# Kernel optimization log

Measured on AMD Instinct MI355X. Metric: run time of the kernel, lower is better.

## Reference

```python
import jax, jax.numpy as jnp
import numpy as np

B = 65536
NQ = 8
NL = 3
FEAT = 64 * 3 * 3 + NQ  # 584


def _conv(x, w, b):
    # x: (B,C,H,W), w: (O,I,3,3), padding=1 -> SAME
    y = jax.lax.conv_general_dilated(
        x, w, window_strides=(1, 1), padding='SAME',
        dimension_numbers=('NCHW', 'OIHW', 'NCHW'))
    return y + b[None, :, None, None]


def _maxpool2(x):
    return jax.lax.reduce_window(
        x, -jnp.inf, jax.lax.max, (1, 1, 2, 2), (1, 1, 2, 2), 'VALID')


def _quantum_sim(x, qp):
    # x: (B,NQ); qp: (NL,NQ,3). Within a layer, qubit q depends only on its own
    # previous state (tanh term), so vectorize over qubits and scan over layers.
    x_next = jnp.roll(x, -1, axis=1)  # x[:, (q+1) % NQ]

    def step(q_state, rot):  # rot: (NQ,3)
        new = jnp.sin(rot[:, 0] * x) * jnp.cos(rot[:, 1] * x_next) \
              + jnp.tanh(rot[:, 2] * q_state)
        return new, None

    q0 = jnp.zeros_like(x)
    qf, _ = jax.lax.scan(step, q0, qp)
    return qf


def setup_inputs() -> dict:
    key = jax.random.key(0)
    ks = jax.random.split(key, 16)

    def w(k, shape, fan_in):
        lim = 1.0 / np.sqrt(fan_in)
        return jax.random.uniform(k, shape, jnp.float32, -lim, lim)

    return {
        'board_state': jax.random.normal(ks[0], (B, 3, 6, 6), jnp.float32),
        'target_positions': jax.random.randint(ks[1], (4, 2), 0, 6).astype(jnp.int64),
        'conv1_w': w(ks[2], (16, 3, 3, 3), 3 * 9), 'conv1_b': w(ks[3], (16,), 3 * 9),
        'conv2_w': w(ks[4], (32, 16, 3, 3), 16 * 9), 'conv2_b': w(ks[5], (32,), 16 * 9),
        'conv3_w': w(ks[6], (64, 32, 3, 3), 32 * 9), 'conv3_b': w(ks[7], (64,), 32 * 9),
        'quantum_params': jax.random.normal(ks[8], (NL, NQ, 3), jnp.float32),
        'pt_w1': w(ks[9], (FEAT, 128), FEAT), 'pt_b1': w(ks[9], (128,), FEAT),
        'pt_w2': w(ks[10], (128, 64), 128), 'pt_b2': w(ks[10], (64,), 128),
        'pt_w3': w(ks[11], (64, 2), 64), 'pt_b3': w(ks[11], (2,), 64),
        'cf_w1': w(ks[12], (FEAT, 64), FEAT), 'cf_b1': w(ks[12], (64,), FEAT),
        'cf_w2': w(ks[13], (64, 1), 64), 'cf_b2': w(ks[13], (1,), 64),
    }


def reference(board_state, target_positions,
              conv1_w, conv1_b, conv2_w, conv2_b, conv3_w, conv3_b,
              quantum_params,
              pt_w1, pt_b1, pt_w2, pt_b2, pt_w3, pt_b3,
              cf_w1, cf_b1, cf_w2, cf_b2):
    b = board_state.shape[0]
    h = jax.nn.relu(_conv(board_state, conv1_w, conv1_b))   # (B,16,6,6)
    h = jax.nn.relu(_conv(h, conv2_w, conv2_b))             # (B,32,6,6)
    h = _maxpool2(h)                                        # (B,32,3,3)
    h = jax.nn.relu(_conv(h, conv3_w, conv3_b))             # (B,64,3,3)
    conv_flat = h.reshape(b, -1)                            # (B,576)

    board_flat = board_state.reshape(b, -1)
    q_feat = _quantum_sim(board_flat[:, :NQ], quantum_params)  # (B,NQ)

    feats = jnp.concatenate([conv_flat, q_feat], axis=1)    # (B,584)

    # piece-type head (Dropout is identity in eval)
    t = jax.nn.relu(feats @ pt_w1 + pt_b1)
    t = jax.nn.relu(t @ pt_w2 + pt_b2)
    type_logits = t @ pt_w3 + pt_b3
    type_probs = jax.nn.softmax(type_logits, axis=1)        # (B,2)

    # confidence head
    c = jax.nn.relu(feats @ cf_w1 + cf_b1)
    confidence = jax.nn.sigmoid(c @ cf_w2 + cf_b2)          # (B,1)

    # target_positions never affect the math (pos_encoding unused in torch source);
    # the same probs/confidence are reported for every position.
    return jnp.concatenate([type_probs, confidence], axis=1)  # (B,3)
```

## Files before the change

### kernel.cpp

```cpp
#include <hip/hip_runtime.h>

typedef _Float16 h8 __attribute__((ext_vector_type(8)));
typedef _Float16 h4 __attribute__((ext_vector_type(4)));
typedef float f32x4 __attribute__((ext_vector_type(4)));

union HU { _Float16 h; unsigned short u; };
__device__ __forceinline__ unsigned short f2h(float f) { HU x; x.h = (_Float16)f; return x.u; }
__device__ __forceinline__ float h2f(unsigned short u) { HU x; x.u = u; return (float)x.h; }

#define MFMA16(a, b, c) __builtin_amdgcn_mfma_f32_16x16x32_f16((a), (b), (c), 0, 0, 0)

__global__ void k_prep(const float* __restrict__ w1, const float* __restrict__ w2,
                       const float* __restrict__ w3,
                       const float* __restrict__ ptw1, const float* __restrict__ cfw1,
                       const float* __restrict__ ptw2, const float* __restrict__ ptw3,
                       const float* __restrict__ cfw2,
                       unsigned short* __restrict__ w1f,
                       unsigned short* __restrict__ w2f,
                       unsigned short* __restrict__ w3f,
                       unsigned short* __restrict__ w1hd,
                       unsigned short* __restrict__ w2hd,
                       unsigned short* __restrict__ w3hd) {
    int gid = blockIdx.x * 256 + threadIdx.x;
    int gs = gridDim.x * 256;
    for (int e = gid; e < 512; e += gs) {
        int j = e & 7, lane = e >> 3;
        int k = ((lane >> 4) * 8) + j, oc = lane & 15;
        float v = 0.f;
        if (k < 27) { int t = k / 3, ic = k % 3; v = w1[oc * 27 + ic * 9 + t]; }
        w1f[e] = f2h(v);
    }
    for (int e = gid; e < 9216; e += gs) {
        int j = e & 7, lane = (e >> 3) & 63, fo = e >> 9;
        int ot = fo & 1, t = fo >> 1;
        int k = ((lane >> 4) * 8) + j, oc = ot * 16 + (lane & 15);
        float v = (k < 16) ? w2[oc * 144 + k * 9 + t] : 0.f;
        w2f[e] = f2h(v);
    }
    for (int e = gid; e < 18432; e += gs) {
        int j = e & 7, lane = (e >> 3) & 63, fo = e >> 9;
        int oti = fo & 1, t = (fo >> 1) % 9, otp = (fo >> 1) / 9;
        int ic = ((lane >> 4) * 8) + j, oc = (otp * 2 + oti) * 16 + (lane & 15);
        w3f[e] = f2h(w3[oc * 288 + ic * 9 + t]);
    }
    for (int s = gid; s < 608 * 192; s += gs) {
        int k = s / 192, n = s - k * 192;
        float v = 0.f;
        if (k < 584) v = (n < 128) ? ptw1[k * 128 + n] : cfw1[k * 64 + (n - 128)];
        int kk = k >> 5, hi = (k & 31) >> 3, j = k & 7, nt = n >> 4;
        int e = (((kk * 12 + nt) << 6) | (hi << 4) | (n & 15)) << 3 | j;
        w1hd[e] = f2h(v);
    }
    for (int s = gid; s < 8192; s += gs) {
        int k = s >> 6, n = s & 63;
        float v = ptw2[k * 64 + n];
        int kk = k >> 5, hi = (k & 31) >> 3, j = k & 7, nt = n >> 4;
        int e = ((((kk << 2) | nt) << 6) | (hi << 4) | (n & 15)) << 3 | j;
        w2hd[e] = f2h(v);
    }
    for (int e = gid; e < 2048; e += gs) {
        int j = e & 7, lane = (e >> 3) & 63, kk = e >> 9;
        int k = kk * 32 + ((lane >> 4) * 8) + j, n = lane & 15;
        float v = 0.f;
        if (k < 64) { if (n < 2) v = ptw3[k * 2 + n]; }
        else        { if (n == 2) v = cfw2[k - 64]; }
        w3hd[e] = f2h(v);
    }
}

#define BDS 194
#define A1S 584
#define A2S 296
#define FTS 616
#define HSH 200
#define RA_OFF 19712
#define O_OFF 26112
#define LDSTOT 26368

template<int PP0, int PP1>
__device__ __forceinline__ void conv2_compute(
    const unsigned short* A1, const h8* W2r, float b2v0, float b2v1,
    int sA1, int q, float pooled[5][2][4])
{
    #pragma unroll
    for (int pi = 0; pi < PP1 - PP0; pi++) {
        const int pp = PP0 + pi;
        #pragma unroll
        for (int sub = 0; sub < 4; sub++) {
            const int y = (pp / 3) * 2 + (sub >> 1), x = (pp % 3) * 2 + (sub & 1);
            f32x4 acc0 = {0.f, 0.f, 0.f, 0.f}, acc1 = {0.f, 0.f, 0.f, 0.f};
            #pragma unroll
            for (int t = 0; t < 9; t++) {
                const int sy = y + t / 3 - 1, sx = x + t % 3 - 1;
                if (sy < 0 || sy >= 6 || sx < 0 || sx >= 6) continue;
                h8 a = *(const h8*)&A1[sA1 + (sy * 6 + sx) * 16 + (q & 1) * 8];
                acc0 = MFMA16(a, W2r[t * 2 + 0], acc0);
                acc1 = MFMA16(a, W2r[t * 2 + 1], acc1);
            }
            #pragma unroll
            for (int r = 0; r < 4; r++) {
                pooled[pi][0][r] = fmaxf(pooled[pi][0][r], acc0[r] + b2v0);
                pooled[pi][1][r] = fmaxf(pooled[pi][1][r], acc1[r] + b2v1);
            }
        }
    }
}

template<int PP0, int PP1>
__device__ __forceinline__ void conv2_store(
    unsigned short* A2, const float pooled[5][2][4], int q, int col)
{
    #pragma unroll
    for (int pi = 0; pi < PP1 - PP0; pi++)
        #pragma unroll
        for (int ot = 0; ot < 2; ot++)
            #pragma unroll
            for (int r = 0; r < 4; r++)
                A2[(q * 4 + r) * A2S + (PP0 + pi) * 32 + ot * 16 + col] =
                    f2h(pooled[pi][ot][r]);
}

__global__ __launch_bounds__(256, 3) void k_fused(
    const float* __restrict__ board,
    const float* __restrict__ b1, const float* __restrict__ b2,
    const float* __restrict__ b3, const float* __restrict__ qp,
    const unsigned short* __restrict__ w1f,
    const unsigned short* __restrict__ w2f,
    const unsigned short* __restrict__ w3f,
    const unsigned short* __restrict__ w1hd,
    const unsigned short* __restrict__ w2hd,
    const unsigned short* __restrict__ w3hd,
    const float* __restrict__ ptb1, const float* __restrict__ ptb2,
    const float* __restrict__ ptb3, const float* __restrict__ cfb1,
    const float* __restrict__ cfb2,
    float* __restrict__ out)
{
    __shared__ __align__(16) unsigned short LDSH[LDSTOT];
    const int tid = threadIdx.x, wid = tid >> 6, lane = tid & 63;
    const int g = wid >> 1, w2 = wid & 1;
    const int col = lane & 15, q = lane >> 4;
    const long long gg0 = (long long)blockIdx.x * 32;
    const f32x4 ZERO4 = {0.f, 0.f, 0.f, 0.f};

    unsigned short* A1 = LDSH + g * 9856;
    unsigned short* A2 = A1;
    unsigned short* Hb = LDSH + RA_OFF;
    float* O = (float*)(LDSH + O_OFF);

    for (int e = tid; e < 1552; e += 256)
        ((unsigned long long*)LDSH)[4928 + e] = 0ULL;
    {
        int g2 = tid >> 7, r = (tid >> 3) & 15, z = tid & 7;
        LDSH[g2 * 9856 + r * A1S + 576 + z] = 0;
    }
    __syncthreads();

    for (int e = tid; e < 32 * 108; e += 256) {
        int ss = e / 108, r2 = e % 108, ch = r2 / 36, p = r2 % 36;
        float v = board[gg0 * 108 + e];
        LDSH[RA_OFF + (ss >> 4) * 3104 + (ss & 15) * BDS +
             ((p / 6 + 1) * 8 + (p % 6) + 1) * 3 + ch] = f2h(v);
    }
    __syncthreads();

    float qv;
    {
        int ss = tid >> 3, qq = tid & 7;
        int base = RA_OFF + (ss >> 4) * 3104 + (ss & 15) * BDS;
        int p8a = ((qq / 6 + 1) * 8 + (qq % 6) + 1) * 3;
        int e2 = (qq + 1) & 7;
        int p8b = ((e2 / 6 + 1) * 8 + (e2 % 6) + 1) * 3;
        float xq = h2f(LDSH[base + p8a]);
        float xn = h2f(LDSH[base + p8b]);
        float st = 0.f;
        for (int l = 0; l < 3; l++) {
            float a0 = qp[l * 24 + qq * 3], a1 = qp[l * 24 + qq * 3 + 1],
                  a2 = qp[l * 24 + qq * 3 + 2];
            st = sinf(a0 * xq) * cosf(a1 * xn) + tanhf(a2 * st);
        }
        qv = st;
    }

    {
        int dlt[8];
        #pragma unroll
        for (int j = 0; j < 8; j++) {
            int k = q * 8 + j;
            if (k < 27) { int t = k / 3, c = k % 3;
                          dlt[j] = ((t / 3 - 1) * 8 + (t % 3 - 1)) * 3 + c; }
            else dlt[j] = 0;
        }
        h8 w1r = ((const h8*)w1f)[lane];
        float b1v = b1[col];
        const int sB = RA_OFF + g * 3104 + col * BDS;
        for (int p = w2 * 18; p < w2 * 18 + 18; p++) {
            int ab = sB + ((p / 6 + 1) * 8 + (p % 6) + 1) * 3;
            union { h8 v; _Float16 e[8]; } af;
            #pragma unroll
            for (int j = 0; j < 8; j++) { HU z; z.u = LDSH[ab + dlt[j]]; af.e[j] = z.h; }
            f32x4 c = MFMA16(af.v, w1r, ZERO4);
            #pragma unroll
            for (int r = 0; r < 4; r++)
                A1[(q * 4 + r) * A1S + p * 16 + col] = f2h(fmaxf(c[r] + b1v, 0.f));
        }
    }
    __syncthreads();

    float pooled[5][2][4];
    #pragma unroll
    for (int pi = 0; pi < 5; pi++)
        #pragma unroll
        for (int ot = 0; ot < 2; ot++)
            #pragma unroll
            for (int r = 0; r < 4; r++) pooled[pi][ot][r] = 0.f;
    {
        h8 W2r[18];
        #pragma unroll
        for (int f = 0; f < 18; f++) W2r[f] = ((const h8*)w2f)[f * 64 + lane];
        float b2v0 = b2[col], b2v1 = b2[16 + col];
        const int sA1 = col * A1S;
        if (w2 == 0) conv2_compute<0, 5>(A1, W2r, b2v0, b2v1, sA1, q, pooled);
        else         conv2_compute<5, 9>(A1, W2r, b2v0, b2v1, sA1, q, pooled);
    }
    __syncthreads();
    if (w2 == 0) conv2_store<0, 5>(A2, pooled, q, col);
    else         conv2_store<5, 9>(A2, pooled, q, col);
    __syncthreads();

    f32x4 c3a[9], c3b[9];
    {
        const int otp = w2;
        const int sA2 = col * A2S;
        h8 W3r[18];
        #pragma unroll
        for (int f = 0; f < 18; f++)
            W3r[f] = ((const h8*)w3f)[(otp * 18 + f) * 64 + lane];
        #pragma unroll
        for (int p = 0; p < 9; p++) {
            const int y = p / 3, x = p % 3;
            f32x4 acc0 = ZERO4, acc1 = ZERO4;
            #pragma unroll
            for (int t = 0; t < 9; t++) {
                const int sy = y + t / 3 - 1, sx = x + t % 3 - 1;
                if (sy < 0 || sy >= 3 || sx < 0 || sx >= 3) continue;
                h8 a = *(const h8*)&A2[sA2 + (sy * 3 + sx) * 32 + q * 8];
                acc0 = MFMA16(a, W3r[t * 2 + 0], acc0);
                acc1 = MFMA16(a, W3r[t * 2 + 1], acc1);
            }
            c3a[p] = acc0; c3b[p] = acc1;
        }
    }
    __syncthreads();

    {
        const int otp = w2;
        float b3v0 = b3[(otp * 2 + 0) * 16 + col];
        float b3v1 = b3[(otp * 2 + 1) * 16 + col];
        int oc0 = (otp * 2 + 0) * 16 + col, oc1 = (otp * 2 + 1) * 16 + col;
        #pragma unroll
        for (int p = 0; p < 9; p++)
            #pragma unroll
            for (int r = 0; r < 4; r++) {
                int row = g * 16 + q * 4 + r;
                LDSH[row * FTS + oc0 * 9 + p] = f2h(fmaxf(c3a[p][r] + b3v0, 0.f));
                LDSH[row * FTS + oc1 * 9 + p] = f2h(fmaxf(c3b[p][r] + b3v1, 0.f));
            }
        LDSH[(tid >> 3) * FTS + 576 + (tid & 7)] = f2h(qv);
        for (int e = tid; e < 1024; e += 256)
            LDSH[(e >> 5) * FTS + 584 + (e & 31)] = 0;
    }
    __syncthreads();

    {
        f32x4 acc[2][3];
        #pragma unroll
        for (int mt = 0; mt < 2; mt++)
            #pragma unroll
            for (int nt = 0; nt < 3; nt++) acc[mt][nt] = ZERO4;
        const h8* wp1 = (const h8*)w1hd;
        const int ntb = wid * 3;
        for (int kk = 0; kk < 19; kk++) {
            h8 a0 = *(const h8*)&LDSH[col * FTS + kk * 32 + q * 8];
            h8 a1 = *(const h8*)&LDSH[(16 + col) * FTS + kk * 32 + q * 8];
            h8 b[3];
            #pragma unroll
            for (int nt = 0; nt < 3; nt++)
                b[nt] = wp1[(kk * 12 + ntb + nt) * 64 + lane];
            #pragma unroll
            for (int nt = 0; nt < 3; nt++) {
                acc[0][nt] = MFMA16(a0, b[nt], acc[0][nt]);
                acc[1][nt] = MFMA16(a1, b[nt], acc[1][nt]);
            }
        }
        #pragma unroll
        for (int nt = 0; nt < 3; nt++) {
            int ntg = ntb + nt;
            float bv = (ntg < 8) ? ptb1[ntg * 16 + col] : cfb1[(ntg - 8) * 16 + col];
            #pragma unroll
            for (int mt = 0; mt < 2; mt++)
                #pragma unroll
                for (int r = 0; r < 4; r++)
                    Hb[(mt * 16 + q * 4 + r) * HSH + ntg * 16 + col] =
                        f2h(fmaxf(acc[mt][nt][r] + bv, 0.f));
        }
    }
    __syncthreads();

    {
        f32x4 acc2[2];
        acc2[0] = ZERO4; acc2[1] = ZERO4;
        const h8* wp2 = (const h8*)w2hd;
        const int nt2 = wid;
        #pragma unroll
        for (int kk = 0; kk < 4; kk++) {
            h8 a0 = *(const h8*)&Hb[col * HSH + kk * 32 + q * 8];
            h8 a1 = *(const h8*)&Hb[(16 + col) * HSH + kk * 32 + q * 8];
            h8 b = wp2[(kk * 4 + nt2) * 64 + lane];
            acc2[0] = MFMA16(a0, b, acc2[0]);
            acc2[1] = MFMA16(a1, b, acc2[1]);
        }
        __syncthreads();
        float bv2 = ptb2[nt2 * 16 + col];
        #pragma unroll
        for (int mt = 0; mt < 2; mt++)
            #pragma unroll
            for (int r = 0; r < 4; r++)
                Hb[(mt * 16 + q * 4 + r) * HSH + nt2 * 16 + col] =
                    f2h(fmaxf(acc2[mt][r] + bv2, 0.f));
    }
    __syncthreads();

    if (wid < 2) {
        const int mt = wid;
        f32x4 a3 = ZERO4;
        #pragma unroll
        for (int kk = 0; kk < 4; kk++) {
            int base = (kk < 2) ? kk * 32 : kk * 32 + 64;
            h8 a = *(const h8*)&Hb[(mt * 16 + col) * HSH + base + q * 8];
            h8 b = ((const h8*)w3hd)[kk * 64 + lane];
            a3 = MFMA16(a, b, a3);
        }
        if (col < 3) {
            float bv = (col < 2) ? ptb3[col] : cfb2[0];
            #pragma unroll
            for (int r = 0; r < 4; r++)
                O[(mt * 16 + q * 4 + r) * 4 + col] = a3[r] + bv;
        }
        if (lane < 16) {
            int s = mt * 16 + lane;
            float l0 = O[s * 4 + 0], l1 = O[s * 4 + 1], l2 = O[s * 4 + 2];
            float m = fmaxf(l0, l1);
            float e0 = expf(l0 - m), e1 = expf(l1 - m);
            float inv = 1.f / (e0 + e1);
            float* op = out + (gg0 + s) * 3;
            op[0] = e0 * inv;
            op[1] = e1 * inv;
            op[2] = 1.f / (1.f + expf(-l2));
        }
    }
}

extern "C" void kernel_launch(void* const* d_in, const int* in_sizes, int n_in,
                              void* d_out, int out_size, void* d_ws, size_t ws_size,
                              hipStream_t stream) {
    const float* board = (const float*)d_in[0];
    const float* c1w  = (const float*)d_in[2];
    const float* c1b  = (const float*)d_in[3];
    const float* c2w  = (const float*)d_in[4];
    const float* c2b  = (const float*)d_in[5];
    const float* c3w  = (const float*)d_in[6];
    const float* c3b  = (const float*)d_in[7];
    const float* qp   = (const float*)d_in[8];
    const float* ptw1 = (const float*)d_in[9];
    const float* ptb1 = (const float*)d_in[10];
    const float* ptw2 = (const float*)d_in[11];
    const float* ptb2 = (const float*)d_in[12];
    const float* ptw3 = (const float*)d_in[13];
    const float* ptb3 = (const float*)d_in[14];
    const float* cfw1 = (const float*)d_in[15];
    const float* cfb1 = (const float*)d_in[16];
    const float* cfw2 = (const float*)d_in[17];
    const float* cfb2 = (const float*)d_in[18];
    float* out = (float*)d_out;

    int Btot = in_sizes[0] / 108;

    unsigned short* w1f   = (unsigned short*)d_ws;
    unsigned short* w2f   = (unsigned short*)((char*)d_ws + 1024);
    unsigned short* w3f   = (unsigned short*)((char*)d_ws + 19456);
    unsigned short* w1hd  = (unsigned short*)((char*)d_ws + 56320);
    unsigned short* w2hd  = (unsigned short*)((char*)d_ws + 289792);
    unsigned short* w3hd  = (unsigned short*)((char*)d_ws + 306176);

    hipLaunchKernelGGL(k_prep, dim3(256), dim3(256), 0, stream,
                       c1w, c2w, c3w, ptw1, cfw1, ptw2, ptw3, cfw2,
                       w1f, w2f, w3f, w1hd, w2hd, w3hd);
    hipLaunchKernelGGL(k_fused, dim3(Btot / 32), dim3(256), 0, stream,
                       board, c1b, c2b, c3b, qp, w1f, w2f, w3f,
                       w1hd, w2hd, w3hd, ptb1, ptb2, ptb3, cfb1, cfb2, out);
}
```

Measured before the change: 189.3 us.

## Repack conv1 input to 4-channel padded layout with vector loads and two MFMAs

The board is now staged in LDS with 4 channel slots per pixel (stride 260), one 16-sample group at a time, so conv1 operands can be fetched as aligned h4 vector loads instead of eight scalar gathers. conv1 becomes two MFMAs (two kernel rows, then the third row) with repacked weights, and all four waves split the pixels of each group. Conv3 features are now written to LDS in position-major order with contiguous channels, and the head weights are permuted to match. The cost is an extra barrier per group, one more MFMA per pixel, and serial processing of the two sample groups for conv1.

```diff
diff --git a/kernel.cpp b/kernel.cpp
--- a/kernel.cpp
+++ b/kernel.cpp
@@ -23,11 +23,15 @@
                        unsigned short* __restrict__ w3hd) {
     int gid = blockIdx.x * 256 + threadIdx.x;
     int gs = gridDim.x * 256;
-    for (int e = gid; e < 512; e += gs) {
-        int j = e & 7, lane = e >> 3;
-        int k = ((lane >> 4) * 8) + j, oc = lane & 15;
+    for (int e = gid; e < 1024; e += gs) {
+        int f = e >> 9, lane = (e >> 3) & 63, j = e & 7;
+        int k = ((lane >> 4) << 3) + j, oc = lane & 15;
+        int r, within;
+        if (f == 0) { r = k >> 4; within = k & 15; }
+        else        { r = 2;      within = k; }
+        int tx = within >> 2, ch = within & 3;
         float v = 0.f;
-        if (k < 27) { int t = k / 3, ic = k % 3; v = w1[oc * 27 + ic * 9 + t]; }
+        if (tx < 3 && ch < 3) v = w1[oc * 27 + ch * 9 + r * 3 + tx];
         w1f[e] = f2h(v);
     }
     for (int e = gid; e < 9216; e += gs) {
@@ -46,7 +50,10 @@
     for (int s = gid; s < 608 * 192; s += gs) {
         int k = s / 192, n = s - k * 192;
         float v = 0.f;
-        if (k < 584) v = (n < 128) ? ptw1[k * 128 + n] : cfw1[k * 64 + (n - 128)];
+        if (k < 584) {
+            int f = (k < 576) ? ((k & 63) * 9 + (k >> 6)) : k;
+            v = (n < 128) ? ptw1[f * 128 + n] : cfw1[f * 64 + (n - 128)];
+        }
         int kk = k >> 5, hi = (k & 31) >> 3, j = k & 7, nt = n >> 4;
         int e = (((kk * 12 + nt) << 6) | (hi << 4) | (n & 15)) << 3 | j;
         w1hd[e] = f2h(v);
@@ -68,7 +75,8 @@
     }
 }
 
-#define BDS 194
+#define BDS4 260
+#define BDH4 (16 * BDS4)
 #define A1S 584
 #define A2S 296
 #define FTS 616
@@ -147,64 +155,62 @@
     unsigned short* Hb = LDSH + RA_OFF;
     float* O = (float*)(LDSH + O_OFF);
 
-    for (int e = tid; e < 1552; e += 256)
-        ((unsigned long long*)LDSH)[4928 + e] = 0ULL;
-    {
-        int g2 = tid >> 7, r = (tid >> 3) & 15, z = tid & 7;
-        LDSH[g2 * 9856 + r * A1S + 576 + z] = 0;
-    }
-    __syncthreads();
-
-    for (int e = tid; e < 32 * 108; e += 256) {
-        int ss = e / 108, r2 = e % 108, ch = r2 / 36, p = r2 % 36;
-        float v = board[gg0 * 108 + e];
-        LDSH[RA_OFF + (ss >> 4) * 3104 + (ss & 15) * BDS +
-             ((p / 6 + 1) * 8 + (p % 6) + 1) * 3 + ch] = f2h(v);
-    }
-    __syncthreads();
-
-    float qv;
-    {
-        int ss = tid >> 3, qq = tid & 7;
-        int base = RA_OFF + (ss >> 4) * 3104 + (ss & 15) * BDS;
-        int p8a = ((qq / 6 + 1) * 8 + (qq % 6) + 1) * 3;
-        int e2 = (qq + 1) & 7;
-        int p8b = ((e2 / 6 + 1) * 8 + (e2 % 6) + 1) * 3;
-        float xq = h2f(LDSH[base + p8a]);
-        float xn = h2f(LDSH[base + p8b]);
-        float st = 0.f;
-        for (int l = 0; l < 3; l++) {
-            float a0 = qp[l * 24 + qq * 3], a1 = qp[l * 24 + qq * 3 + 1],
-                  a2 = qp[l * 24 + qq * 3 + 2];
-            st = sinf(a0 * xq) * cosf(a1 * xn) + tanhf(a2 * st);
-        }
-        qv = st;
-    }
-
-    {
-        int dlt[8];
-        #pragma unroll
-        for (int j = 0; j < 8; j++) {
-            int k = q * 8 + j;
-            if (k < 27) { int t = k / 3, c = k % 3;
-                          dlt[j] = ((t / 3 - 1) * 8 + (t % 3 - 1)) * 3 + c; }
-            else dlt[j] = 0;
-        }
-        h8 w1r = ((const h8*)w1f)[lane];
-        float b1v = b1[col];
-        const int sB = RA_OFF + g * 3104 + col * BDS;
-        for (int p = w2 * 18; p < w2 * 18 + 18; p++) {
-            int ab = sB + ((p / 6 + 1) * 8 + (p % 6) + 1) * 3;
-            union { h8 v; _Float16 e[8]; } af;
-            #pragma unroll
-            for (int j = 0; j < 8; j++) { HU z; z.u = LDSH[ab + dlt[j]]; af.e[j] = z.h; }
-            f32x4 c = MFMA16(af.v, w1r, ZERO4);
-            #pragma unroll
-            for (int r = 0; r < 4; r++)
-                A1[(q * 4 + r) * A1S + p * 16 + col] = f2h(fmaxf(c[r] + b1v, 0.f));
-        }
-    }
-    __syncthreads();
+    for (int e = tid; e < BDH4 / 4; e += 256)
+        ((unsigned long long*)(LDSH + RA_OFF))[e] = 0ULL;
+    __syncthreads();
+
+    float qv[2];
+    h8 w1r0 = ((const h8*)w1f)[lane];
+    h8 w1r1 = ((const h8*)w1f)[64 + lane];
+    float b1v = b1[col];
+    #pragma unroll
+    for (int gi = 0; gi < 2; gi++) {
+        for (int e = tid; e < 16 * 108; e += 256) {
+            int ss = e / 108, r2 = e % 108, ch = r2 / 36, p = r2 % 36;
+            float v = board[(gg0 + gi * 16) * 108 + e];
+            LDSH[RA_OFF + ss * BDS4 + ((p / 6 + 1) * 8 + (p % 6) + 1) * 4 + ch] =
+                f2h(v);
+        }
+        __syncthreads();
+        if (tid < 128) {
+            int ss = tid >> 3, qq = tid & 7;
+            int base = RA_OFF + ss * BDS4;
+            int p8a = ((qq / 6 + 1) * 8 + (qq % 6) + 1) * 4;
+            int e2 = (qq + 1) & 7;
+            int p8b = ((e2 / 6 + 1) * 8 + (e2 % 6) + 1) * 4;
+            float xq = h2f(LDSH[base + p8a]);
+            float xn = h2f(LDSH[base + p8b]);
+            float st = 0.f;
+            for (int l = 0; l < 3; l++) {
+                float a0 = qp[l * 24 + qq * 3], a1 = qp[l * 24 + qq * 3 + 1],
+                      a2 = qp[l * 24 + qq * 3 + 2];
+                st = sinf(a0 * xq) * cosf(a1 * xn) + tanhf(a2 * st);
+            }
+            qv[gi] = st;
+        }
+        {
+            unsigned short* A1g = LDSH + gi * 9856;
+            const int bs = RA_OFF + col * BDS4;
+            const int rsel = q >> 1, wo = (q & 1) * 8;
+            for (int p = wid * 9; p < wid * 9 + 9; p++) {
+                int y = p / 6, x = p % 6;
+                int ab1 = bs + ((y + rsel) * 8 + x) * 4 + wo;
+                int ab2 = bs + ((y + 2) * 8 + x) * 4 + wo;
+                union { h8 v; h4 h[2]; } a1v, a2v;
+                a1v.h[0] = *(const h4*)&LDSH[ab1];
+                a1v.h[1] = *(const h4*)&LDSH[ab1 + 4];
+                a2v.h[0] = *(const h4*)&LDSH[ab2];
+                a2v.h[1] = *(const h4*)&LDSH[ab2 + 4];
+                f32x4 c = MFMA16(a1v.v, w1r0, ZERO4);
+                c = MFMA16(a2v.v, w1r1, c);
+                #pragma unroll
+                for (int r = 0; r < 4; r++)
+                    A1g[(q * 4 + r) * A1S + p * 16 + col] =
+                        f2h(fmaxf(c[r] + b1v, 0.f));
+            }
+        }
+        __syncthreads();
+    }
 
     float pooled[5][2][4];
     #pragma unroll
@@ -262,10 +268,14 @@
             #pragma unroll
             for (int r = 0; r < 4; r++) {
                 int row = g * 16 + q * 4 + r;
-                LDSH[row * FTS + oc0 * 9 + p] = f2h(fmaxf(c3a[p][r] + b3v0, 0.f));
-                LDSH[row * FTS + oc1 * 9 + p] = f2h(fmaxf(c3b[p][r] + b3v1, 0.f));
-            }
-        LDSH[(tid >> 3) * FTS + 576 + (tid & 7)] = f2h(qv);
+                LDSH[row * FTS + p * 64 + oc0] = f2h(fmaxf(c3a[p][r] + b3v0, 0.f));
+                LDSH[row * FTS + p * 64 + oc1] = f2h(fmaxf(c3b[p][r] + b3v1, 0.f));
+            }
+        if (tid < 128) {
+            int ss = tid >> 3, qq = tid & 7;
+            LDSH[ss * FTS + 576 + qq] = f2h(qv[0]);
+            LDSH[(ss + 16) * FTS + 576 + qq] = f2h(qv[1]);
+        }
         for (int e = tid; e < 1024; e += 256)
             LDSH[(e >> 5) * FTS + 584 + (e & 31)] = 0;
     }
@@ -386,11 +396,11 @@
     int Btot = in_sizes[0] / 108;
 
     unsigned short* w1f   = (unsigned short*)d_ws;
-    unsigned short* w2f   = (unsigned short*)((char*)d_ws + 1024);
-    unsigned short* w3f   = (unsigned short*)((char*)d_ws + 19456);
-    unsigned short* w1hd  = (unsigned short*)((char*)d_ws + 56320);
-    unsigned short* w2hd  = (unsigned short*)((char*)d_ws + 289792);
-    unsigned short* w3hd  = (unsigned short*)((char*)d_ws + 306176);
+    unsigned short* w2f   = (unsigned short*)((char*)d_ws + 2048);
+    unsigned short* w3f   = (unsigned short*)((char*)d_ws + 20480);
+    unsigned short* w1hd  = (unsigned short*)((char*)d_ws + 57344);
+    unsigned short* w2hd  = (unsigned short*)((char*)d_ws + 290816);
+    unsigned short* w3hd  = (unsigned short*)((char*)d_ws + 307200);
 
     hipLaunchKernelGGL(k_prep, dim3(256), dim3(256), 0, stream,
                        c1w, c2w, c3w, ptw1, cfw1, ptw2, ptw3, cfw2,
```

Result: faster. 181.3 us (-4.2%).
